# Kernel tuning notes

Measured on AMD Instinct MI355X. Metric: run time of the kernel, lower is better.

The kernel has to match this reference:

```python
import jax, jax.numpy as jnp
from jax import lax
import numpy as np

HIDDEN = 32


def setup_inputs() -> dict:
    key = jax.random.key(0)
    ks = jax.random.split(key, 7)
    B, T = 4096, 512
    s = 1.0 / np.sqrt(HIDDEN)  # PyTorch default uniform init bound
    x = jax.random.normal(ks[0], (B, T), dtype=jnp.float32)
    W_ih = jax.random.uniform(ks[1], (4 * HIDDEN, 1), jnp.float32, -s, s)
    W_hh = jax.random.uniform(ks[2], (4 * HIDDEN, HIDDEN), jnp.float32, -s, s)
    b_ih = jax.random.uniform(ks[3], (4 * HIDDEN,), jnp.float32, -s, s)
    b_hh = jax.random.uniform(ks[4], (4 * HIDDEN,), jnp.float32, -s, s)
    W_fc = jax.random.uniform(ks[5], (1, HIDDEN), jnp.float32, -s, s)
    b_fc = jax.random.uniform(ks[6], (1,), jnp.float32, -s, s)
    return {"x": x, "W_ih": W_ih, "W_hh": W_hh, "b_ih": b_ih,
            "b_hh": b_hh, "W_fc": W_fc, "b_fc": b_fc}


def reference(x, W_ih, W_hh, b_ih, b_hh, W_fc, b_fc):
    B, T = x.shape
    H = HIDDEN
    # input projection is time-parallel: precompute x_t * W_ih + biases -> [T, B, 4H]
    x_proj = x.T[:, :, None] * W_ih[:, 0][None, None, :] + (b_ih + b_hh)

    def step(carry, xp):
        h, c = carry
        gates = xp + h @ W_hh.T                      # [B, 4H]
        i, f, g, o = jnp.split(gates, 4, axis=-1)    # PyTorch gate order i,f,g,o
        i = jax.nn.sigmoid(i)
        f = jax.nn.sigmoid(f)
        g = jnp.tanh(g)
        o = jax.nn.sigmoid(o)
        c = f * c + i * g
        h = o * jnp.tanh(c)
        return (h, c), None

    h0 = jnp.zeros((B, H), x.dtype)
    c0 = jnp.zeros((B, H), x.dtype)
    (h_last, _), _ = lax.scan(step, (h0, c0), x_proj)
    return h_last @ W_fc.T + b_fc                    # [B, 1]
```

## Files before the change

kernel.cpp:

```cpp
#include <hip/hip_runtime.h>


static constexpr int T_LEN = 512;
static constexpr int H = 32;

typedef _Float16 h2   __attribute__((ext_vector_type(2)));
typedef __fp16   fp2  __attribute__((ext_vector_type(2)));
typedef _Float16 v8h  __attribute__((ext_vector_type(8)));
typedef float    v4f  __attribute__((ext_vector_type(4)));

__device__ __forceinline__ v4f MF32(v8h a, v8h b, v4f c) {
#if __has_builtin(__builtin_amdgcn_mfma_f32_16x16x32_f16)
    return __builtin_amdgcn_mfma_f32_16x16x32_f16(a, b, c, 0, 0, 0);
#else
    v4f d = c;
    asm("v_mfma_f32_16x16x32_f16 %0, %1, %2, %0" : "+v"(d) : "v"(a), "v"(b));
    return d;
#endif
}

__device__ __forceinline__ v8h mkB(uint4 w) {
    union { uint4 u; v8h v; } u;
    u.u = w; return u.v;
}

__global__ void
__attribute__((amdgpu_flat_work_group_size(128, 128), amdgpu_waves_per_eu(1, 1)))
reslstm_kernel(const float* __restrict__ x,
               const float* __restrict__ W_ih,
               const float* __restrict__ W_hh,
               const float* __restrict__ b_ih,
               const float* __restrict__ b_hh,
               const float* __restrict__ W_fc,
               const float* __restrict__ b_fc,
               float* __restrict__ out, int B)
{
    __shared__ float xl[16][36];
    __shared__ uint2 hx[2][4][16][2];
    __shared__ float osum[2][16];

    const int tid  = threadIdx.x;
    const int lane = tid & 63;
    const int wv   = tid >> 6;
    const int c    = lane & 15;
    const int q    = lane >> 4;

    const int wbase = blockIdx.x << 4;
    if (wbase >= B) return;
    const int bb = wbase + c;

    constexpr float NL2E  = -1.4426950408889634f;
    constexpr float N2L2E = 2.0f * NL2E;

    v8h A8[4];
    v4f wih[4], bsb[4];
    #pragma unroll
    for (int k = 0; k < 4; ++k) {
        const int   t  = 2 * k + wv;
        const float sc = (k == 2) ? N2L2E : NL2E;
        const float4 w1 = *reinterpret_cast<const float4*>(
            W_hh + (16 * t + c) * H + 4 * q);
        const float4 w2 = *reinterpret_cast<const float4*>(
            W_hh + (16 * t + c) * H + 16 + 4 * q);
        A8[k][0] = (_Float16)(w1.x * sc); A8[k][1] = (_Float16)(w1.y * sc);
        A8[k][2] = (_Float16)(w1.z * sc); A8[k][3] = (_Float16)(w1.w * sc);
        A8[k][4] = (_Float16)(w2.x * sc); A8[k][5] = (_Float16)(w2.y * sc);
        A8[k][6] = (_Float16)(w2.z * sc); A8[k][7] = (_Float16)(w2.w * sc);
        const int r0 = 16 * t + 4 * q;
        const float4 wi = *reinterpret_cast<const float4*>(W_ih + r0);
        const float4 bi = *reinterpret_cast<const float4*>(b_ih + r0);
        const float4 bh = *reinterpret_cast<const float4*>(b_hh + r0);
        wih[k][0] = wi.x * sc; wih[k][1] = wi.y * sc;
        wih[k][2] = wi.z * sc; wih[k][3] = wi.w * sc;
        bsb[k][0] = (bi.x + bh.x) * sc; bsb[k][1] = (bi.y + bh.y) * sc;
        bsb[k][2] = (bi.z + bh.z) * sc; bsb[k][3] = (bi.w + bh.w) * sc;
    }

    float cs0 = 0.f, cs1 = 0.f, cs2 = 0.f, cs3 = 0.f;
    float hv0 = 0.f, hv1 = 0.f, hv2 = 0.f, hv3 = 0.f;
    v8h B8 = mkB(uint4{0u, 0u, 0u, 0u});

#define PINALL()                                                              \
    asm volatile("" : "+v"(A8[0]), "+v"(A8[1]), "+v"(A8[2]), "+v"(A8[3]));    \
    asm volatile("" : "+v"(wih[0]), "+v"(wih[1]), "+v"(wih[2]), "+v"(wih[3]), \
                      "+v"(bsb[0]), "+v"(bsb[1]), "+v"(bsb[2]), "+v"(bsb[3]))

#define GSTATE(AI, AF, AG, AO, CC, HH) do {                                   \
    const float Ei = __builtin_amdgcn_exp2f(AI);                              \
    const float Ef = __builtin_amdgcn_exp2f(AF);                              \
    const float Eg = __builtin_amdgcn_exp2f(AG);                              \
    const float Eo = __builtin_amdgcn_exp2f(AO);                              \
    const float Di = 1.0f + Ei, Df = 1.0f + Ef;                               \
    const float Dg = 1.0f + Eg, Do_ = 1.0f + Eo;                              \
    const float P  = Di * Dg;                                                 \
    const float t_ = (1.0f - Eg) * Df;                                        \
    const float u_ = __builtin_fmaf(CC, P, t_);                               \
    const float Rc = __builtin_amdgcn_rcpf(Df * P);                           \
    CC = u_ * Rc;                                                             \
    const float Ec = __builtin_amdgcn_exp2f(CC * N2L2E);                      \
    const float Dc = 1.0f + Ec;                                               \
    const float Rh = __builtin_amdgcn_rcpf(Do_ * Dc);                         \
    HH = (1.0f - Ec) * Rh;                                                    \
} while (0)

#define STEP(XT, PAR) do {                                                    \
    const float xt = (XT);                                                    \
    v4f acc[4];                                                               \
    _Pragma("unroll")                                                         \
    for (int k = 0; k < 4; ++k) acc[k] = bsb[k] + wih[k] * xt;                \
    _Pragma("unroll")                                                         \
    for (int k = 0; k < 4; ++k) acc[k] = MF32(A8[k], B8, acc[k]);             \
    unsigned int* slot =                                                      \
        reinterpret_cast<unsigned int*>(&hx[PAR][q][c][wv]);                  \
    GSTATE(acc[0][0], acc[1][0], acc[2][0], acc[3][0], cs0, hv0);             \
    GSTATE(acc[0][1], acc[1][1], acc[2][1], acc[3][1], cs1, hv1);             \
    slot[0] = __builtin_bit_cast(unsigned int,                                \
                  __builtin_amdgcn_cvt_pkrtz(hv0, hv1));                      \
    GSTATE(acc[0][2], acc[1][2], acc[2][2], acc[3][2], cs2, hv2);             \
    GSTATE(acc[0][3], acc[1][3], acc[2][3], acc[3][3], cs3, hv3);             \
    slot[1] = __builtin_bit_cast(unsigned int,                                \
                  __builtin_amdgcn_cvt_pkrtz(hv2, hv3));                      \
    asm volatile("s_waitcnt lgkmcnt(0)\n\ts_barrier" ::: "memory");           \
    B8 = mkB(*reinterpret_cast<const uint4*>(&hx[PAR][q][c][0]));             \
} while (0)

    const int r    = tid >> 3;
    const int colb = (tid & 7) << 2;
    const float* xsrc = x + (size_t)(wbase + r) * T_LEN + colb;
    float4 xA = *reinterpret_cast<const float4*>(xsrc);

    for (int tc = 0; tc < T_LEN / 32; ++tc) {
        PINALL();
        *reinterpret_cast<float4*>(&xl[r][colb]) = xA;
        __syncthreads();
        if (tc + 1 < T_LEN / 32)
            xA = *reinterpret_cast<const float4*>(xsrc + (tc + 1) * 32);
        const float4* xq4c = reinterpret_cast<const float4*>(&xl[c][0]);
        #pragma unroll 2
        for (int t4 = 0; t4 < 8; ++t4) {
            const float4 xv = xq4c[t4];
            STEP(xv.x, 0);
            STEP(xv.y, 1);
            STEP(xv.z, 0);
            STEP(xv.w, 1);
        }
    }
#undef STEP
#undef GSTATE
#undef PINALL

    const int u0 = 16 * wv + 4 * q;
    float val = hv0 * W_fc[u0]     + hv1 * W_fc[u0 + 1]
              + hv2 * W_fc[u0 + 2] + hv3 * W_fc[u0 + 3];
    val += __shfl_xor(val, 16);
    val += __shfl_xor(val, 32);
    if (q == 0) osum[wv][c] = val;
    __syncthreads();
    if (wv == 0 && q == 0 && bb < B)
        out[bb] = osum[0][c] + osum[1][c] + b_fc[0];
}

extern "C" void kernel_launch(void* const* d_in, const int* in_sizes, int n_in,
                              void* d_out, int out_size, void* d_ws, size_t ws_size,
                              hipStream_t stream) {
    const float* x    = (const float*)d_in[0];
    const float* W_ih = (const float*)d_in[1];
    const float* W_hh = (const float*)d_in[2];
    const float* b_ih = (const float*)d_in[3];
    const float* b_hh = (const float*)d_in[4];
    const float* W_fc = (const float*)d_in[5];
    const float* b_fc = (const float*)d_in[6];
    float* out = (float*)d_out;
    const int B = in_sizes[0] / T_LEN;
    dim3 block(128);
    dim3 grid((B + 15) / 16);
    reslstm_kernel<<<grid, block, 0, stream>>>(x, W_ih, W_hh, b_ih, b_hh,
                                               W_fc, b_fc, out, B);
}
```

Baseline: 239.9 us.

## Pack four independent 16-row batch groups into one 512-thread block

Each block now processes 64 batch rows as four independent 2-wave groups, cutting the grid from 256 to 64 blocks and raising waves_per_eu to 2. The intent is to put two waves per SIMD so the serial recurrence latency of one group can overlap with another group's work. In exchange, the per-step s_barrier now synchronises all 8 waves in the block, so every group stalls on the slowest one, and fewer blocks are spread across the CUs.

After: 326.2 us. +36.0%, slower.

```diff
diff --git a/kernel.cpp b/kernel.cpp
--- a/kernel.cpp
+++ b/kernel.cpp
@@ -25,7 +25,7 @@
 }
 
 __global__ void
-__attribute__((amdgpu_flat_work_group_size(128, 128), amdgpu_waves_per_eu(1, 1)))
+__attribute__((amdgpu_flat_work_group_size(512, 512), amdgpu_waves_per_eu(2, 2)))
 reslstm_kernel(const float* __restrict__ x,
                const float* __restrict__ W_ih,
                const float* __restrict__ W_hh,
@@ -35,19 +35,22 @@
                const float* __restrict__ b_fc,
                float* __restrict__ out, int B)
 {
-    __shared__ float xl[16][36];
-    __shared__ uint2 hx[2][4][16][2];
-    __shared__ float osum[2][16];
+    __shared__ float xl[4][16][36];
+    __shared__ uint2 hx[4][2][4][16][2];
+    __shared__ float osum[4][2][16];
 
     const int tid  = threadIdx.x;
     const int lane = tid & 63;
     const int wv   = tid >> 6;
+    const int grp  = wv >> 1;
+    const int wp   = wv & 1;
     const int c    = lane & 15;
     const int q    = lane >> 4;
 
-    const int wbase = blockIdx.x << 4;
+    const int wbase = blockIdx.x << 6;
     if (wbase >= B) return;
-    const int bb = wbase + c;
+    const int bbase = wbase + (grp << 4);
+    const int bb    = bbase + c;
 
     constexpr float NL2E  = -1.4426950408889634f;
     constexpr float N2L2E = 2.0f * NL2E;
@@ -56,7 +59,7 @@
     v4f wih[4], bsb[4];
     #pragma unroll
     for (int k = 0; k < 4; ++k) {
-        const int   t  = 2 * k + wv;
+        const int   t  = 2 * k + wp;
         const float sc = (k == 2) ? N2L2E : NL2E;
         const float4 w1 = *reinterpret_cast<const float4*>(
             W_hh + (16 * t + c) * H + 4 * q);
@@ -111,7 +114,7 @@
     _Pragma("unroll")                                                         \
     for (int k = 0; k < 4; ++k) acc[k] = MF32(A8[k], B8, acc[k]);             \
     unsigned int* slot =                                                      \
-        reinterpret_cast<unsigned int*>(&hx[PAR][q][c][wv]);                  \
+        reinterpret_cast<unsigned int*>(&hx[grp][PAR][q][c][wp]);             \
     GSTATE(acc[0][0], acc[1][0], acc[2][0], acc[3][0], cs0, hv0);             \
     GSTATE(acc[0][1], acc[1][1], acc[2][1], acc[3][1], cs1, hv1);             \
     slot[0] = __builtin_bit_cast(unsigned int,                                \
@@ -121,21 +124,22 @@
     slot[1] = __builtin_bit_cast(unsigned int,                                \
                   __builtin_amdgcn_cvt_pkrtz(hv2, hv3));                      \
     asm volatile("s_waitcnt lgkmcnt(0)\n\ts_barrier" ::: "memory");           \
-    B8 = mkB(*reinterpret_cast<const uint4*>(&hx[PAR][q][c][0]));             \
+    B8 = mkB(*reinterpret_cast<const uint4*>(&hx[grp][PAR][q][c][0]));        \
 } while (0)
 
-    const int r    = tid >> 3;
-    const int colb = (tid & 7) << 2;
-    const float* xsrc = x + (size_t)(wbase + r) * T_LEN + colb;
+    const int sg    = tid >> 7;
+    const int sr    = (tid >> 3) & 15;
+    const int scolb = (tid & 7) << 2;
+    const float* xsrc = x + (size_t)(wbase + (sg << 4) + sr) * T_LEN + scolb;
     float4 xA = *reinterpret_cast<const float4*>(xsrc);
 
     for (int tc = 0; tc < T_LEN / 32; ++tc) {
         PINALL();
-        *reinterpret_cast<float4*>(&xl[r][colb]) = xA;
+        *reinterpret_cast<float4*>(&xl[sg][sr][scolb]) = xA;
         __syncthreads();
         if (tc + 1 < T_LEN / 32)
             xA = *reinterpret_cast<const float4*>(xsrc + (tc + 1) * 32);
-        const float4* xq4c = reinterpret_cast<const float4*>(&xl[c][0]);
+        const float4* xq4c = reinterpret_cast<const float4*>(&xl[grp][c][0]);
         #pragma unroll 2
         for (int t4 = 0; t4 < 8; ++t4) {
             const float4 xv = xq4c[t4];
@@ -149,15 +153,15 @@
 #undef GSTATE
 #undef PINALL
 
-    const int u0 = 16 * wv + 4 * q;
+    const int u0 = 16 * wp + 4 * q;
     float val = hv0 * W_fc[u0]     + hv1 * W_fc[u0 + 1]
               + hv2 * W_fc[u0 + 2] + hv3 * W_fc[u0 + 3];
     val += __shfl_xor(val, 16);
     val += __shfl_xor(val, 32);
-    if (q == 0) osum[wv][c] = val;
+    if (q == 0) osum[grp][wp][c] = val;
     __syncthreads();
-    if (wv == 0 && q == 0 && bb < B)
-        out[bb] = osum[0][c] + osum[1][c] + b_fc[0];
+    if (wp == 0 && q == 0 && bb < B)
+        out[bb] = osum[grp][0][c] + osum[grp][1][c] + b_fc[0];
 }
 
 extern "C" void kernel_launch(void* const* d_in, const int* in_sizes, int n_in,
@@ -172,8 +176,8 @@
     const float* b_fc = (const float*)d_in[6];
     float* out = (float*)d_out;
     const int B = in_sizes[0] / T_LEN;
-    dim3 block(128);
-    dim3 grid((B + 15) / 16);
+    dim3 block(512);
+    dim3 grid((B + 63) / 64);
     reslstm_kernel<<<grid, block, 0, stream>>>(x, W_ih, W_hh, b_ih, b_hh,
                                                W_fc, b_fc, out, B);
 }
```
